# Kernel tuning notes

Hardware: AMD Instinct MI355X
Metric: run time of the kernel (lower is better)

Reference implementation:

```python
import jax, jax.numpy as jnp
import numpy as np

N = 50000       # nodes
E = 600000      # edges
C_IN, C_HID, C_OUT = 128, 128, 40


def setup_inputs() -> dict:
    key = jax.random.key(0)
    k0, k1, k2, k3 = jax.random.split(key, 4)
    x = jax.random.normal(k0, (N, C_IN), dtype=jnp.float32)
    edge_index = jax.random.randint(k1, (2, E), 0, N)
    s1 = 1.0 / np.sqrt(C_IN)
    W1 = jax.random.uniform(k2, (C_IN, C_HID), jnp.float32, -s1, s1)
    b1 = jnp.zeros((C_HID,), jnp.float32)
    s2 = 1.0 / np.sqrt(C_HID)
    W2 = jax.random.uniform(k3, (C_HID, C_OUT), jnp.float32, -s2, s2)
    b2 = jnp.zeros((C_OUT,), jnp.float32)
    return {"x": x, "edge_index": edge_index, "W1": W1, "b1": b1, "W2": W2, "b2": b2}


def gcn_conv(x, W, b, src, dst, n):
    """PyG GCNConv: add self-loops, symmetric D^-1/2 A D^-1/2 aggregation."""
    h = x @ W  # [N, C_out]
    ones = jnp.ones(src.shape[0], dtype=h.dtype)
    # degree at target nodes including the self-loop (+1)
    deg = jax.ops.segment_sum(ones, dst, num_segments=n) + 1.0
    dinv = jax.lax.rsqrt(deg)                       # deg >= 1, no inf
    norm = dinv[src] * dinv[dst]                    # [E]
    agg = jax.ops.segment_sum(h[src] * norm[:, None], dst, num_segments=n)
    agg = agg + h * (dinv * dinv)[:, None]          # self-loop contribution
    return agg + b


def reference(x, edge_index, W1, b1, W2, b2):
    src, dst = edge_index[0], edge_index[1]
    h = gcn_conv(x, W1, b1, src, dst, N)
    h = jax.nn.relu(h)
    # F.dropout(training=self.training): identity in eval/inference mode
    return gcn_conv(h, W2, b2, src, dst, N)
```

## Files before the change

### kernel.cpp

```cpp
#include <hip/hip_runtime.h>


#define CAPC 48

typedef __attribute__((ext_vector_type(8))) short bf16x8;
typedef __attribute__((ext_vector_type(4))) float f32x4;

__device__ inline unsigned short f2bf(float x) {
    unsigned u = __float_as_uint(x);
    unsigned r = (u + 0x7FFFu + ((u >> 16) & 1u)) >> 16;
    return (unsigned short)r;
}
__device__ inline float bflo(unsigned u) { return __uint_as_float(u << 16); }
__device__ inline float bfhi(unsigned u) { return __uint_as_float(u & 0xFFFF0000u); }

__device__ inline void fma8(float* acc, uint4 uv, float wt) {
    acc[0] = fmaf(bflo(uv.x), wt, acc[0]);
    acc[1] = fmaf(bfhi(uv.x), wt, acc[1]);
    acc[2] = fmaf(bflo(uv.y), wt, acc[2]);
    acc[3] = fmaf(bfhi(uv.y), wt, acc[3]);
    acc[4] = fmaf(bflo(uv.z), wt, acc[4]);
    acc[5] = fmaf(bfhi(uv.z), wt, acc[5]);
    acc[6] = fmaf(bflo(uv.w), wt, acc[6]);
    acc[7] = fmaf(bfhi(uv.w), wt, acc[7]);
}

__global__ __launch_bounds__(256) void k_zero(int* __restrict__ cnt,
                                              int* __restrict__ ovcnt,
                                              const float* __restrict__ W1,
                                              const float* __restrict__ W2,
                                              unsigned short* __restrict__ WT,
                                              unsigned short* __restrict__ WT2,
                                              int n, int nb) {
    int b = blockIdx.x;
    if (b < nb) {
        int i = b * 256 + threadIdx.x;
        if (i < n) cnt[i] = 0;
        if (b == 0 && threadIdx.x == 0) *ovcnt = 0;
    } else if (b < nb + 16) {
        int idx = (b - nb) * 256 + threadIdx.x;
        for (int i = idx; i < 128 * 128; i += 4096) {
            int k = i >> 7, c = i & 127;
            WT[c * 128 + k] = f2bf(W1[i]);
        }
    } else {
        int idx = (b - nb - 16) * 256 + threadIdx.x;
        for (int i = idx; i < 48 * 128; i += 2048) {
            int c = i >> 7, k = i & 127;
            WT2[i] = (c < 40) ? f2bf(W2[k * 40 + c]) : (unsigned short)0;
        }
    }
}

__global__ __launch_bounds__(256) void k_scatter(const int* __restrict__ src,
                                                 const int* __restrict__ dst,
                                                 int* __restrict__ cnt,
                                                 int* __restrict__ esrcb,
                                                 int2* __restrict__ ovbuf,
                                                 int* __restrict__ ovcnt, int m) {
    int e = blockIdx.x * 256 + threadIdx.x;
    if (e >= m) return;
    int s = src[e], d = dst[e];
    int pos = atomicAdd(&cnt[d], 1);
    if (pos < CAPC) {
        esrcb[(size_t)d * CAPC + pos] = s;
    } else {
        int o = atomicAdd(ovcnt, 1);
        ovbuf[o] = make_int2(d, s);
    }
}

__global__ __launch_bounds__(256) void k_gemm1(
    const float* __restrict__ X, const unsigned short* __restrict__ WT,
    unsigned short* __restrict__ Hb, const int* __restrict__ cnt,
    float* __restrict__ dinv, int n, int ngb)
{
    if (blockIdx.x >= ngb) {
        int i = (blockIdx.x - ngb) * 256 + threadIdx.x;
        if (i < n) dinv[i] = rsqrtf((float)cnt[i] + 1.0f);
        return;
    }

    const int l  = threadIdx.x & 63;
    const int w  = threadIdx.x >> 6;
    const int rw = blockIdx.x * 64 + w * 16;
    const int lr = l & 15;
    const int kq = l >> 4;

    int arow = rw + lr;
    if (arow > n - 1) arow = n - 1;
    const float* xp = X + (size_t)arow * 128 + kq * 8;

    f32x4 acc[8];
#pragma unroll
    for (int j = 0; j < 8; ++j) acc[j] = (f32x4){0.f, 0.f, 0.f, 0.f};

#pragma unroll
    for (int kk = 0; kk < 4; ++kk) {
        float4 v0 = *(const float4*)(xp + kk * 32);
        float4 v1 = *(const float4*)(xp + kk * 32 + 4);
        bf16x8 a;
        a[0] = (short)f2bf(v0.x); a[1] = (short)f2bf(v0.y);
        a[2] = (short)f2bf(v0.z); a[3] = (short)f2bf(v0.w);
        a[4] = (short)f2bf(v1.x); a[5] = (short)f2bf(v1.y);
        a[6] = (short)f2bf(v1.z); a[7] = (short)f2bf(v1.w);
#pragma unroll
        for (int j = 0; j < 8; ++j) {
            const bf16x8 b = *(const bf16x8*)(WT + (size_t)(j * 16 + lr) * 128 + kk * 32 + kq * 8);
            acc[j] = __builtin_amdgcn_mfma_f32_16x16x32_bf16(a, b, acc[j], 0, 0, 0);
        }
    }

#pragma unroll
    for (int j = 0; j < 8; ++j) {
        int col = j * 16 + lr;
#pragma unroll
        for (int r4 = 0; r4 < 4; ++r4) {
            int rr = rw + kq * 4 + r4;
            if (rr < n) Hb[(size_t)rr * 128 + col] = f2bf(acc[j][r4]);
        }
    }
}

__global__ __launch_bounds__(256) void k_agg1g2(
    const int* __restrict__ cnt, const int* __restrict__ esrcb,
    const int2* __restrict__ ovbuf, const int* __restrict__ ovcnt,
    const unsigned short* __restrict__ Hb, const float* __restrict__ B1,
    const unsigned short* __restrict__ WT2, const float* __restrict__ dinv,
    unsigned short* __restrict__ H3b, int n)
{
    __shared__ unsigned short tile[64][132];
    const int t  = threadIdx.x;
    const int r0 = blockIdx.x * 64;
    const int lane = t & 15;
    const int slot = t >> 4;
    const int ovn  = *ovcnt;

    for (int rr = slot; rr < 64; rr += 16) {
        int r = r0 + rr;
        if (r < n) {
            float dd = dinv[r], d2 = dd * dd;
            uint4 hu = *(const uint4*)&Hb[(size_t)r * 128 + lane * 8];
            float a0[8], a1[8] = {}, a2[8] = {}, a3[8] = {};
            {
                const float* bp = &B1[lane * 8];
                float h[8] = {bflo(hu.x), bfhi(hu.x), bflo(hu.y), bfhi(hu.y),
                              bflo(hu.z), bfhi(hu.z), bflo(hu.w), bfhi(hu.w)};
#pragma unroll
                for (int c = 0; c < 8; ++c) a0[c] = fmaf(h[c], d2, bp[c]);
            }
            int deg = cnt[r];
            int cap = deg < CAPC ? deg : CAPC;
            const int* ep = esrcb + (size_t)r * CAPC;
            int j = 0;
            for (; j + 4 <= cap; j += 4) {
                int s0 = ep[j], s1 = ep[j + 1], s2 = ep[j + 2], s3 = ep[j + 3];
                uint4 u0 = *(const uint4*)&Hb[(size_t)s0 * 128 + lane * 8];
                uint4 u1 = *(const uint4*)&Hb[(size_t)s1 * 128 + lane * 8];
                uint4 u2 = *(const uint4*)&Hb[(size_t)s2 * 128 + lane * 8];
                uint4 u3 = *(const uint4*)&Hb[(size_t)s3 * 128 + lane * 8];
                fma8(a0, u0, dinv[s0] * dd);
                fma8(a1, u1, dinv[s1] * dd);
                fma8(a2, u2, dinv[s2] * dd);
                fma8(a3, u3, dinv[s3] * dd);
            }
            for (; j < cap; ++j) {
                int s0 = ep[j];
                uint4 u = *(const uint4*)&Hb[(size_t)s0 * 128 + lane * 8];
                fma8(a0, u, dinv[s0] * dd);
            }
            if (ovn > 0) {
                for (int k = 0; k < ovn; ++k) {
                    int2 e = ovbuf[k];
                    if (e.x == r) {
                        uint4 u = *(const uint4*)&Hb[(size_t)e.y * 128 + lane * 8];
                        fma8(a0, u, dinv[e.y] * dd);
                    }
                }
            }
            unsigned o[4];
#pragma unroll
            for (int c = 0; c < 4; ++c) {
                float lo = fmaxf(a0[2*c]   + a1[2*c]   + a2[2*c]   + a3[2*c],   0.f);
                float hi = fmaxf(a0[2*c+1] + a1[2*c+1] + a2[2*c+1] + a3[2*c+1], 0.f);
                o[c] = (unsigned)f2bf(lo) | ((unsigned)f2bf(hi) << 16);
            }
            *(uint4*)&tile[rr][lane * 8] = make_uint4(o[0], o[1], o[2], o[3]);
        }
    }
    __syncthreads();

    const int l  = t & 63;
    const int w  = t >> 6;
    const int rw = r0 + w * 16;
    const int lr = l & 15;
    const int kq = l >> 4;

    f32x4 acc[3];
#pragma unroll
    for (int j = 0; j < 3; ++j) acc[j] = (f32x4){0.f, 0.f, 0.f, 0.f};

#pragma unroll
    for (int kk = 0; kk < 4; ++kk) {
        const bf16x8 a = *(const bf16x8*)&tile[w * 16 + lr][kk * 32 + kq * 8];
#pragma unroll
        for (int j = 0; j < 3; ++j) {
            const bf16x8 b = *(const bf16x8*)(WT2 + (size_t)(j * 16 + lr) * 128 + kk * 32 + kq * 8);
            acc[j] = __builtin_amdgcn_mfma_f32_16x16x32_bf16(a, b, acc[j], 0, 0, 0);
        }
    }

#pragma unroll
    for (int j = 0; j < 3; ++j) {
        int col = j * 16 + lr;
        if (col < 40) {
#pragma unroll
            for (int r4 = 0; r4 < 4; ++r4) {
                int rr = rw + kq * 4 + r4;
                if (rr < n) H3b[(size_t)rr * 40 + col] = f2bf(acc[j][r4]);
            }
        }
    }
}

__global__ __launch_bounds__(320) void k_agg2(
    const int* __restrict__ cnt, const int* __restrict__ esrcb,
    const int2* __restrict__ ovbuf, const int* __restrict__ ovcnt,
    const unsigned short* __restrict__ H3b, const float* __restrict__ B,
    const float* __restrict__ dinv, float* __restrict__ OUT, int n)
{
    int t = threadIdx.x;
    int r = blockIdx.x * 64 + t / 5;
    int q = t % 5;
    if (r >= n) return;
    float dd = dinv[r], d2 = dd * dd;
    uint4 hu = *(const uint4*)&H3b[(size_t)r * 40 + q * 8];
    float a0[8], a1[8] = {}, a2[8] = {}, a3[8] = {};
    {
        const float* bp = &B[q * 8];
        float h[8] = {bflo(hu.x), bfhi(hu.x), bflo(hu.y), bfhi(hu.y),
                      bflo(hu.z), bfhi(hu.z), bflo(hu.w), bfhi(hu.w)};
#pragma unroll
        for (int c = 0; c < 8; ++c) a0[c] = fmaf(h[c], d2, bp[c]);
    }
    int deg = cnt[r];
    int cap = deg < CAPC ? deg : CAPC;
    const int* ep = esrcb + (size_t)r * CAPC;
    int j = 0;
    for (; j + 4 <= cap; j += 4) {
        int s0 = ep[j], s1 = ep[j + 1], s2 = ep[j + 2], s3 = ep[j + 3];
        uint4 u0 = *(const uint4*)&H3b[(size_t)s0 * 40 + q * 8];
        uint4 u1 = *(const uint4*)&H3b[(size_t)s1 * 40 + q * 8];
        uint4 u2 = *(const uint4*)&H3b[(size_t)s2 * 40 + q * 8];
        uint4 u3 = *(const uint4*)&H3b[(size_t)s3 * 40 + q * 8];
        fma8(a0, u0, dinv[s0] * dd);
        fma8(a1, u1, dinv[s1] * dd);
        fma8(a2, u2, dinv[s2] * dd);
        fma8(a3, u3, dinv[s3] * dd);
    }
    for (; j < cap; ++j) {
        int s0 = ep[j];
        uint4 u = *(const uint4*)&H3b[(size_t)s0 * 40 + q * 8];
        fma8(a0, u, dinv[s0] * dd);
    }
    int ovn = *ovcnt;
    if (ovn > 0) {
        for (int k = 0; k < ovn; ++k) {
            int2 e = ovbuf[k];
            if (e.x == r) {
                uint4 u = *(const uint4*)&H3b[(size_t)e.y * 40 + q * 8];
                fma8(a0, u, dinv[e.y] * dd);
            }
        }
    }
    float o[8];
#pragma unroll
    for (int c = 0; c < 8; ++c) o[c] = a0[c] + a1[c] + a2[c] + a3[c];
    float* p = &OUT[(size_t)r * 40 + q * 8];
    *(float4*)(p)     = make_float4(o[0], o[1], o[2], o[3]);
    *(float4*)(p + 4) = make_float4(o[4], o[5], o[6], o[7]);
}

extern "C" void kernel_launch(void* const* d_in, const int* in_sizes, int n_in,
                              void* d_out, int out_size, void* d_ws, size_t ws_size,
                              hipStream_t stream) {
    const float* x  = (const float*)d_in[0];
    const int*   ei = (const int*)d_in[1];
    const float* W1 = (const float*)d_in[2];
    const float* b1 = (const float*)d_in[3];
    const float* W2 = (const float*)d_in[4];
    const float* b2 = (const float*)d_in[5];
    float* out = (float*)d_out;

    const int n = in_sizes[0] / 128;
    const int m = in_sizes[1] / 2;
    const int* src = ei;
    const int* dst = ei + m;
    const int nb  = (n + 255) / 256;
    const int ngb = (n + 63) / 64;

    char* p = (char*)d_ws;
    auto take = [&](size_t bytes) { char* q = p; p += (bytes + 255) & ~(size_t)255; return q; };
    int*   cnt    = (int*)take(sizeof(int) * n);
    int*   ovcnt  = (int*)take(sizeof(int) * 64);
    int2*  ovbuf  = (int2*)take(sizeof(int2) * 8192);
    int*   esrcb  = (int*)take(sizeof(int) * (size_t)n * CAPC);
    float* dinv   = (float*)take(sizeof(float) * n);
    unsigned short* WT  = (unsigned short*)take(sizeof(short) * 128 * 128);
    unsigned short* WT2 = (unsigned short*)take(sizeof(short) * 48 * 128);
    unsigned short* H1b = (unsigned short*)take(sizeof(short) * (size_t)n * 128);
    unsigned short* H3b = (unsigned short*)take(sizeof(short) * (size_t)n * 40);

    k_zero   <<<nb + 24, 256, 0, stream>>>(cnt, ovcnt, W1, W2, WT, WT2, n, nb);
    k_scatter<<<(m + 255) / 256, 256, 0, stream>>>(src, dst, cnt, esrcb, ovbuf, ovcnt, m);
    k_gemm1  <<<ngb + nb, 256, 0, stream>>>(x, WT, H1b, cnt, dinv, n, ngb);
    k_agg1g2 <<<ngb, 256, 0, stream>>>(cnt, esrcb, ovbuf, ovcnt, H1b, b1, WT2, dinv, H3b, n);
    k_agg2   <<<(n + 63) / 64, 320, 0, stream>>>(cnt, esrcb, ovbuf, ovcnt, H3b, b2, dinv, out, n);
}
```

Baseline: 119.7 us.

## Fuse edge scatter into GEMM1 launch and recompute dinv from counts on the fly

The edge-bucketing scatter now runs as extra blocks of the first GEMM kernel instead of its own launch, so the independent GEMM and scatter work can overlap in one launch. The dinv array is removed, and each aggregation kernel recomputes rsqrt(deg+1) from the count array for every gathered neighbour. This drops one kernel launch and the dinv write/read pass. In exchange it adds an rsqrt per gathered edge, and the scatter atomics now contend with GEMM blocks.

```diff
diff --git a/kernel.cpp b/kernel.cpp
--- a/kernel.cpp
+++ b/kernel.cpp
@@ -13,6 +13,7 @@
 }
 __device__ inline float bflo(unsigned u) { return __uint_as_float(u << 16); }
 __device__ inline float bfhi(unsigned u) { return __uint_as_float(u & 0xFFFF0000u); }
+__device__ inline float dinv_of(int deg) { return rsqrtf((float)deg + 1.0f); }
 
 __device__ inline void fma8(float* acc, uint4 uv, float wt) {
     acc[0] = fmaf(bflo(uv.x), wt, acc[0]);
@@ -52,32 +53,26 @@
     }
 }
 
-__global__ __launch_bounds__(256) void k_scatter(const int* __restrict__ src,
-                                                 const int* __restrict__ dst,
-                                                 int* __restrict__ cnt,
-                                                 int* __restrict__ esrcb,
-                                                 int2* __restrict__ ovbuf,
-                                                 int* __restrict__ ovcnt, int m) {
-    int e = blockIdx.x * 256 + threadIdx.x;
-    if (e >= m) return;
-    int s = src[e], d = dst[e];
-    int pos = atomicAdd(&cnt[d], 1);
-    if (pos < CAPC) {
-        esrcb[(size_t)d * CAPC + pos] = s;
-    } else {
-        int o = atomicAdd(ovcnt, 1);
-        ovbuf[o] = make_int2(d, s);
-    }
-}
-
-__global__ __launch_bounds__(256) void k_gemm1(
+__global__ __launch_bounds__(256) void k_gemm1sc(
     const float* __restrict__ X, const unsigned short* __restrict__ WT,
-    unsigned short* __restrict__ Hb, const int* __restrict__ cnt,
-    float* __restrict__ dinv, int n, int ngb)
+    unsigned short* __restrict__ Hb,
+    const int* __restrict__ src, const int* __restrict__ dst,
+    int* __restrict__ cnt, int* __restrict__ esrcb,
+    int2* __restrict__ ovbuf, int* __restrict__ ovcnt,
+    int n, int m, int ngb)
 {
     if (blockIdx.x >= ngb) {
-        int i = (blockIdx.x - ngb) * 256 + threadIdx.x;
-        if (i < n) dinv[i] = rsqrtf((float)cnt[i] + 1.0f);
+        int e = (blockIdx.x - ngb) * 256 + threadIdx.x;
+        if (e < m) {
+            int s = src[e], d = dst[e];
+            int pos = atomicAdd(&cnt[d], 1);
+            if (pos < CAPC) {
+                esrcb[(size_t)d * CAPC + pos] = s;
+            } else {
+                int o = atomicAdd(ovcnt, 1);
+                ovbuf[o] = make_int2(d, s);
+            }
+        }
         return;
     }
 
@@ -126,7 +121,7 @@
     const int* __restrict__ cnt, const int* __restrict__ esrcb,
     const int2* __restrict__ ovbuf, const int* __restrict__ ovcnt,
     const unsigned short* __restrict__ Hb, const float* __restrict__ B1,
-    const unsigned short* __restrict__ WT2, const float* __restrict__ dinv,
+    const unsigned short* __restrict__ WT2,
     unsigned short* __restrict__ H3b, int n)
 {
     __shared__ unsigned short tile[64][132];
@@ -139,7 +134,8 @@
     for (int rr = slot; rr < 64; rr += 16) {
         int r = r0 + rr;
         if (r < n) {
-            float dd = dinv[r], d2 = dd * dd;
+            int deg = cnt[r];
+            float dd = dinv_of(deg), d2 = dd * dd;
             uint4 hu = *(const uint4*)&Hb[(size_t)r * 128 + lane * 8];
             float a0[8], a1[8] = {}, a2[8] = {}, a3[8] = {};
             {
@@ -149,7 +145,6 @@
 #pragma unroll
                 for (int c = 0; c < 8; ++c) a0[c] = fmaf(h[c], d2, bp[c]);
             }
-            int deg = cnt[r];
             int cap = deg < CAPC ? deg : CAPC;
             const int* ep = esrcb + (size_t)r * CAPC;
             int j = 0;
@@ -159,22 +154,22 @@
                 uint4 u1 = *(const uint4*)&Hb[(size_t)s1 * 128 + lane * 8];
                 uint4 u2 = *(const uint4*)&Hb[(size_t)s2 * 128 + lane * 8];
                 uint4 u3 = *(const uint4*)&Hb[(size_t)s3 * 128 + lane * 8];
-                fma8(a0, u0, dinv[s0] * dd);
-                fma8(a1, u1, dinv[s1] * dd);
-                fma8(a2, u2, dinv[s2] * dd);
-                fma8(a3, u3, dinv[s3] * dd);
+                fma8(a0, u0, dinv_of(cnt[s0]) * dd);
+                fma8(a1, u1, dinv_of(cnt[s1]) * dd);
+                fma8(a2, u2, dinv_of(cnt[s2]) * dd);
+                fma8(a3, u3, dinv_of(cnt[s3]) * dd);
             }
             for (; j < cap; ++j) {
                 int s0 = ep[j];
                 uint4 u = *(const uint4*)&Hb[(size_t)s0 * 128 + lane * 8];
-                fma8(a0, u, dinv[s0] * dd);
+                fma8(a0, u, dinv_of(cnt[s0]) * dd);
             }
             if (ovn > 0) {
                 for (int k = 0; k < ovn; ++k) {
                     int2 e = ovbuf[k];
                     if (e.x == r) {
                         uint4 u = *(const uint4*)&Hb[(size_t)e.y * 128 + lane * 8];
-                        fma8(a0, u, dinv[e.y] * dd);
+                        fma8(a0, u, dinv_of(cnt[e.y]) * dd);
                     }
                 }
             }
@@ -227,13 +222,14 @@
     const int* __restrict__ cnt, const int* __restrict__ esrcb,
     const int2* __restrict__ ovbuf, const int* __restrict__ ovcnt,
     const unsigned short* __restrict__ H3b, const float* __restrict__ B,
-    const float* __restrict__ dinv, float* __restrict__ OUT, int n)
+    float* __restrict__ OUT, int n)
 {
     int t = threadIdx.x;
     int r = blockIdx.x * 64 + t / 5;
     int q = t % 5;
     if (r >= n) return;
-    float dd = dinv[r], d2 = dd * dd;
+    int deg = cnt[r];
+    float dd = dinv_of(deg), d2 = dd * dd;
     uint4 hu = *(const uint4*)&H3b[(size_t)r * 40 + q * 8];
     float a0[8], a1[8] = {}, a2[8] = {}, a3[8] = {};
     {
@@ -243,7 +239,6 @@
 #pragma unroll
         for (int c = 0; c < 8; ++c) a0[c] = fmaf(h[c], d2, bp[c]);
     }
-    int deg = cnt[r];
     int cap = deg < CAPC ? deg : CAPC;
     const int* ep = esrcb + (size_t)r * CAPC;
     int j = 0;
@@ -253,15 +248,15 @@
         uint4 u1 = *(const uint4*)&H3b[(size_t)s1 * 40 + q * 8];
         uint4 u2 = *(const uint4*)&H3b[(size_t)s2 * 40 + q * 8];
         uint4 u3 = *(const uint4*)&H3b[(size_t)s3 * 40 + q * 8];
-        fma8(a0, u0, dinv[s0] * dd);
-        fma8(a1, u1, dinv[s1] * dd);
-        fma8(a2, u2, dinv[s2] * dd);
-        fma8(a3, u3, dinv[s3] * dd);
+        fma8(a0, u0, dinv_of(cnt[s0]) * dd);
+        fma8(a1, u1, dinv_of(cnt[s1]) * dd);
+        fma8(a2, u2, dinv_of(cnt[s2]) * dd);
+        fma8(a3, u3, dinv_of(cnt[s3]) * dd);
     }
     for (; j < cap; ++j) {
         int s0 = ep[j];
         uint4 u = *(const uint4*)&H3b[(size_t)s0 * 40 + q * 8];
-        fma8(a0, u, dinv[s0] * dd);
+        fma8(a0, u, dinv_of(cnt[s0]) * dd);
     }
     int ovn = *ovcnt;
     if (ovn > 0) {
@@ -269,7 +264,7 @@
             int2 e = ovbuf[k];
             if (e.x == r) {
                 uint4 u = *(const uint4*)&H3b[(size_t)e.y * 40 + q * 8];
-                fma8(a0, u, dinv[e.y] * dd);
+                fma8(a0, u, dinv_of(cnt[e.y]) * dd);
             }
         }
     }
@@ -298,6 +293,7 @@
     const int* dst = ei + m;
     const int nb  = (n + 255) / 256;
     const int ngb = (n + 63) / 64;
+    const int nsb = (m + 255) / 256;
 
     char* p = (char*)d_ws;
     auto take = [&](size_t bytes) { char* q = p; p += (bytes + 255) & ~(size_t)255; return q; };
@@ -305,15 +301,14 @@
     int*   ovcnt  = (int*)take(sizeof(int) * 64);
     int2*  ovbuf  = (int2*)take(sizeof(int2) * 8192);
     int*   esrcb  = (int*)take(sizeof(int) * (size_t)n * CAPC);
-    float* dinv   = (float*)take(sizeof(float) * n);
     unsigned short* WT  = (unsigned short*)take(sizeof(short) * 128 * 128);
     unsigned short* WT2 = (unsigned short*)take(sizeof(short) * 48 * 128);
     unsigned short* H1b = (unsigned short*)take(sizeof(short) * (size_t)n * 128);
     unsigned short* H3b = (unsigned short*)take(sizeof(short) * (size_t)n * 40);
 
     k_zero   <<<nb + 24, 256, 0, stream>>>(cnt, ovcnt, W1, W2, WT, WT2, n, nb);
-    k_scatter<<<(m + 255) / 256, 256, 0, stream>>>(src, dst, cnt, esrcb, ovbuf, ovcnt, m);
-    k_gemm1  <<<ngb + nb, 256, 0, stream>>>(x, WT, H1b, cnt, dinv, n, ngb);
-    k_agg1g2 <<<ngb, 256, 0, stream>>>(cnt, esrcb, ovbuf, ovcnt, H1b, b1, WT2, dinv, H3b, n);
-    k_agg2   <<<(n + 63) / 64, 320, 0, stream>>>(cnt, esrcb, ovbuf, ovcnt, H3b, b2, dinv, out, n);
-}
+    k_gemm1sc<<<ngb + nsb, 256, 0, stream>>>(x, WT, H1b, src, dst, cnt,
+                                             esrcb, ovbuf, ovcnt, n, m, ngb);
+    k_agg1g2 <<<ngb, 256, 0, stream>>>(cnt, esrcb, ovbuf, ovcnt, H1b, b1, WT2, H3b, n);
+    k_agg2   <<<(n + 63) / 64, 320, 0, stream>>>(cnt, esrcb, ovbuf, ovcnt, H3b, b2, out, n);
+}
```

Result: no change. 121.4 us (+1.4%).
